# Kernel tuning notes

Hardware: AMD Instinct MI355X
Metric: run time of the kernel (lower is better)

The kernel has to match this reference:

```python
import jax, jax.numpy as jnp
import numpy as np

N_NODES = 50000
N_EDGES = 1600000
CHANNELS = 128
EXPANSION = 50
CUTOFF = 5.0
LOG2 = 0.6931471805599453


def shifted_softplus(x):
    return jax.nn.softplus(x) - LOG2


def gaussian_smearing(r, cutoff=CUTOFF, n=EXPANSION):
    # centers evenly spaced in [0, cutoff]; width set by spacing
    centers = jnp.linspace(0.0, cutoff, n, dtype=r.dtype)
    delta = centers[1] - centers[0]
    coef = 1.0 / (2.0 * delta * delta)
    d = r[:, None] - centers[None, :]          # [E, n]
    return jnp.exp(-coef * d * d)


def setup_inputs() -> dict:
    key = jax.random.key(0)
    ks = jax.random.split(key, 12)
    C, F = CHANNELS, EXPANSION

    def lin(k, fan_in, shape):
        bound = 1.0 / np.sqrt(fan_in)
        return jax.random.uniform(k, shape, jnp.float32, -bound, bound)

    return {
        "features": jax.random.normal(ks[0], (N_NODES, C), jnp.float32),
        "edge_distances": jax.random.uniform(ks[1], (N_EDGES,), jnp.float32) * CUTOFF,
        "W_lin": lin(ks[2], C, (C, C)),
        "Wf1": lin(ks[3], F, (F, C)), "bf1": lin(ks[4], F, (C,)),
        "Wf2": lin(ks[5], C, (C, C)), "bf2": lin(ks[6], C, (C,)),
        "Wm1": lin(ks[7], C, (C, C)), "bm1": lin(ks[8], C, (C,)),
        "Wm2": lin(ks[9], C, (C, C)), "bm2": lin(ks[10], C, (C,)),
        "senders": jax.random.randint(ks[11], (N_EDGES,), 0, N_NODES, jnp.int32),
        "receivers": jax.random.randint(jax.random.fold_in(key, 99), (N_EDGES,), 0, N_NODES, jnp.int32),
    }


def reference(features, edge_distances, W_lin, Wf1, bf1, Wf2, bf2,
              Wm1, bm1, Wm2, bm2, senders, receivers):
    # 1. linear transform of node features (no bias)
    h = features @ W_lin.T                                   # [N, C]
    # 2. learnable radial filter F(r_ij): Gaussian basis -> MLP
    basis = gaussian_smearing(edge_distances)                # [E, F]
    ef = shifted_softplus(basis @ Wf1 + bf1) @ Wf2 + bf2     # [E, C]
    # 3. gather neighbour features, elementwise multiply, scatter-sum
    messages = h[senders] * ef                               # [E, C]
    agg = jax.ops.segment_sum(messages, receivers, num_segments=N_NODES)  # [N, C]
    # 4. output MLP
    return shifted_softplus(agg @ Wm1 + bm1) @ Wm2 + bm2
```

## Files before the change

kernel.cpp:

```cpp
#include <hip/hip_runtime.h>
#include <hip/hip_bf16.h>
#include <math.h>

#define N_NODES 50000
#define N_EDGES 1600000
#define CH 128
#define NF 50
#define NR 16384
#define NODES_PER_BLK 8
#define CHUNK 1024
#define NB 512
#define BUCKET_NODES 98
#define CAP 3840
#define PASSA_CHUNK 4096
#define NBLK_SCAT 391
#define NBLK_TB   8192
#define NBLK_DH   782

constexpr float DELTA  = 5.0f / 49.0f;
constexpr float COEF   = 1.0f / (2.0f * DELTA * DELTA);
constexpr float LOG2_  = 0.6931471805599453f;
constexpr float RSCALE = (float)(NR - 1) / 5.0f;

typedef short  bf16x8 __attribute__((ext_vector_type(8)));
typedef float  f32x4  __attribute__((ext_vector_type(4)));
typedef unsigned short ushort_t;
typedef unsigned long long u64;

__device__ __forceinline__ float ssp(float x) {
    return fmaxf(x, 0.0f) + __logf(1.0f + __expf(-fabsf(x))) - LOG2_;
}
__device__ __forceinline__ ushort_t f2bf(float x) {
    __hip_bfloat16 b = __float2bfloat16(x);
    return *reinterpret_cast<ushort_t*>(&b);
}
__device__ __forceinline__ float bf2f(ushort_t u) {
    return __uint_as_float(((unsigned)u) << 16);
}
__device__ __forceinline__ float4 f4zero() { return make_float4(0.f, 0.f, 0.f, 0.f); }

__global__ __launch_bounds__(256) void k1_prep(const float* __restrict__ Wlin,
                                               const float* __restrict__ Wm1,
                                               const float* __restrict__ Wm2,
                                               ushort_t* __restrict__ wlhi,
                                               ushort_t* __restrict__ wllo,
                                               ushort_t* __restrict__ wm1hi,
                                               ushort_t* __restrict__ wm1lo,
                                               ushort_t* __restrict__ wm2hi,
                                               ushort_t* __restrict__ wm2lo,
                                               int* __restrict__ bcnt) {
    const int tid = threadIdx.x;
    if (blockIdx.x == 64) {
        bcnt[tid] = 0;
        bcnt[tid + 256] = 0;
        return;
    }
    int idx = blockIdx.x * 256 + tid;
    int n = idx >> 7, k = idx & 127;
    {   float w = Wlin[(size_t)n * CH + k];
        ushort_t hi = f2bf(w); wlhi[n * CH + k] = hi; wllo[n * CH + k] = f2bf(w - bf2f(hi)); }
    {   float w = Wm1[(size_t)k * CH + n];
        ushort_t hi = f2bf(w); wm1hi[n * CH + k] = hi; wm1lo[n * CH + k] = f2bf(w - bf2f(hi)); }
    {   float w = Wm2[(size_t)k * CH + n];
        ushort_t hi = f2bf(w); wm2hi[n * CH + k] = hi; wm2lo[n * CH + k] = f2bf(w - bf2f(hi)); }
}

__device__ void scatter_body(char* smem, int blk,
                             const int* __restrict__ recv,
                             const int* __restrict__ send,
                             const float* __restrict__ dist,
                             int* __restrict__ bcnt,
                             u64* __restrict__ brec) {
    int* bcur   = (int*)smem;
    int* bbaseL = bcur + NB;
    const int tid = threadIdx.x;
    for (int i = tid; i < NB; i += 256) bcur[i] = 0;
    __syncthreads();
    const int e0 = blk * PASSA_CHUNK;
#pragma unroll
    for (int i = 0; i < 16; i++) {
        int e = e0 + tid + i * 256;
        if (e < N_EDGES) atomicAdd(&bcur[recv[e] / BUCKET_NODES], 1);
    }
    __syncthreads();
    for (int i = tid; i < NB; i += 256) {
        int c = bcur[i];
        bbaseL[i] = c ? atomicAdd(&bcnt[i], c) : 0;
        bcur[i] = 0;
    }
    __syncthreads();
#pragma unroll
    for (int i = 0; i < 16; i++) {
        int e = e0 + tid + i * 256;
        if (e < N_EDGES) {
            int r = recv[e];
            int b = r / BUCKET_NODES;
            int rank = bbaseL[b] + atomicAdd(&bcur[b], 1);
            if (rank < CAP) {
                float x = fminf(dist[e] * RSCALE, (float)(NR - 1));
                int ti = __float2int_rn(x);
                u64 rec = (u64)(unsigned)(send[e] | (r << 16)) | ((u64)ti << 32);
                brec[(size_t)b * CAP + rank] = rec;
            }
        }
    }
}

__device__ void table_body(char* smem, int blk,
                           const float* __restrict__ Wf1,
                           const float* __restrict__ bf1,
                           const float* __restrict__ Wf2,
                           const float* __restrict__ bf2,
                           ushort_t* __restrict__ tabn) {
    float* bas = (float*)smem;
    float* t1  = (float*)smem + 128;
    const int tid  = threadIdx.x;
    const int half = tid >> 7, t = tid & 127;
    const int g = blk * 2 + half;
    const float r = (float)g * (5.0f / (float)(NR - 1));
    if (t < 64) {
        float v = 0.f;
        if (t < NF) { float d = r - (float)t * DELTA; v = __expf(-COEF * d * d); }
        bas[half * 64 + t] = v;
    }
    __syncthreads();
    float acc = bf1[t];
    for (int k = 0; k < NF; k++) acc = fmaf(bas[half * 64 + k], Wf1[k * CH + t], acc);
    t1[half * 128 + t] = ssp(acc);
    __syncthreads();
    float acc2 = bf2[t];
    for (int k = 0; k < CH; k++) acc2 = fmaf(t1[half * 128 + k], Wf2[k * CH + t], acc2);
    tabn[(size_t)g * CH + t] = f2bf(acc2);
}

__device__ void dense_h_body(char* smem, int blk,
                             const float* __restrict__ X,
                             const ushort_t* __restrict__ Bhi,
                             const ushort_t* __restrict__ Blo,
                             ushort_t* __restrict__ Y) {
    ushort_t (*xs)[136] = (ushort_t (*)[136])smem;
    const int tid  = threadIdx.x;
    const int row0 = blk * 64;

#pragma unroll
    for (int i = 0; i < 8; i++) {
        int idx = tid + i * 256;
        int r   = idx >> 5;
        int c4  = (idx & 31) * 4;
        float4 v = (row0 + r < N_NODES) ? *(const float4*)&X[(size_t)(row0 + r) * CH + c4]
                                        : f4zero();
        ushort4 s;
        s.x = f2bf(v.x); s.y = f2bf(v.y); s.z = f2bf(v.z); s.w = f2bf(v.w);
        *(ushort4*)&xs[r][c4] = s;
    }
    __syncthreads();

    const int lane = tid & 63;
    const int wv   = tid >> 6;
    const int row  = lane & 15;
    const int quad = lane >> 4;
    const int c0   = (2 * wv) * 16 + row;
    const int c1   = c0 + 16;

    f32x4 acc[2][4];
#pragma unroll
    for (int j = 0; j < 2; j++)
#pragma unroll
        for (int rt = 0; rt < 4; rt++) acc[j][rt] = (f32x4){0.f, 0.f, 0.f, 0.f};

#pragma unroll
    for (int kb = 0; kb < 128; kb += 32) {
        bf16x8 B0h = *(const bf16x8*)&Bhi[(size_t)c0 * CH + kb + quad * 8];
        bf16x8 B0l = *(const bf16x8*)&Blo[(size_t)c0 * CH + kb + quad * 8];
        bf16x8 B1h = *(const bf16x8*)&Bhi[(size_t)c1 * CH + kb + quad * 8];
        bf16x8 B1l = *(const bf16x8*)&Blo[(size_t)c1 * CH + kb + quad * 8];
#pragma unroll
        for (int rt = 0; rt < 4; rt++) {
            bf16x8 A = *(const bf16x8*)&xs[rt * 16 + row][kb + quad * 8];
            acc[0][rt] = __builtin_amdgcn_mfma_f32_16x16x32_bf16(A, B0l, acc[0][rt], 0, 0, 0);
            acc[0][rt] = __builtin_amdgcn_mfma_f32_16x16x32_bf16(A, B0h, acc[0][rt], 0, 0, 0);
            acc[1][rt] = __builtin_amdgcn_mfma_f32_16x16x32_bf16(A, B1l, acc[1][rt], 0, 0, 0);
            acc[1][rt] = __builtin_amdgcn_mfma_f32_16x16x32_bf16(A, B1h, acc[1][rt], 0, 0, 0);
        }
    }

#pragma unroll
    for (int j = 0; j < 2; j++) {
        int c = j ? c1 : c0;
#pragma unroll
        for (int rt = 0; rt < 4; rt++)
#pragma unroll
            for (int rg = 0; rg < 4; rg++) {
                int r = row0 + rt * 16 + quad * 4 + rg;
                if (r < N_NODES) Y[(size_t)r * CH + c] = f2bf(acc[j][rt][rg]);
            }
    }
}

__global__ __launch_bounds__(256) void k2_mega(const int* __restrict__ recv,
                                               const int* __restrict__ send,
                                               const float* __restrict__ dist,
                                               int* __restrict__ bcnt,
                                               u64* __restrict__ brec,
                                               const float* __restrict__ Wf1,
                                               const float* __restrict__ bf1,
                                               const float* __restrict__ Wf2,
                                               const float* __restrict__ bf2,
                                               ushort_t* __restrict__ tabn,
                                               const float* __restrict__ X,
                                               const ushort_t* __restrict__ wlhi,
                                               const ushort_t* __restrict__ wllo,
                                               ushort_t* __restrict__ h) {
    __shared__ __align__(16) char smem[64 * 136 * 2];
    const int blk = blockIdx.x;
    if (blk < NBLK_SCAT) {
        scatter_body(smem, blk, recv, send, dist, bcnt, brec);
    } else if (blk < NBLK_SCAT + NBLK_TB) {
        table_body(smem, blk - NBLK_SCAT, Wf1, bf1, Wf2, bf2, tabn);
    } else {
        dense_h_body(smem, blk - NBLK_SCAT - NBLK_TB, X, wlhi, wllo, h);
    }
}

__global__ __launch_bounds__(256) void bucket_sort(const int* __restrict__ bcnt,
                                                   const u64* __restrict__ brec,
                                                   unsigned* __restrict__ meta,
                                                   int* __restrict__ cursor) {
    __shared__ int sbc[NB];
    __shared__ int shist[BUCKET_NODES];
    __shared__ int sexc[BUCKET_NODES];
    __shared__ unsigned sout[CAP];
    __shared__ int sgb;
    const int b = blockIdx.x, tid = threadIdx.x;
    const int nbase = b * BUCKET_NODES;
    const int nn = min(BUCKET_NODES, N_NODES - nbase);
    if (nn <= 0) return;

    sbc[tid] = bcnt[tid];
    sbc[tid + 256] = bcnt[tid + 256];
    for (int i = tid; i < nn; i += 256) shist[i] = 0;
    __syncthreads();
    if (tid == 0) {
        int acc = 0;
        for (int i = 0; i < b; i++) acc += min(sbc[i], CAP);
        sgb = acc;
    }
    __syncthreads();
    const int gbase = sgb;
    const int m = min(sbc[b], CAP);
    const u64* my = brec + (size_t)b * CAP;

    for (int i = tid; i < m; i += 256) {
        int l = (int)((my[i] >> 16) & 0xFFFF) - nbase;
        atomicAdd(&shist[l], 1);
    }
    __syncthreads();
    if (tid == 0) {
        int acc = 0;
        for (int l = 0; l < nn; l++) { sexc[l] = acc; acc += shist[l]; }
    }
    __syncthreads();
    for (int l = tid; l < nn; l += 256)
        cursor[nbase + l] = gbase + sexc[l] + shist[l];
    __syncthreads();
    for (int i = tid; i < m; i += 256) {
        u64 rec = my[i];
        int l = (int)((rec >> 16) & 0xFFFF) - nbase;
        int rank = atomicAdd(&sexc[l], 1);
        sout[rank] = (unsigned)(rec & 0xFFFF) | ((unsigned)((rec >> 32) & 0x3FFF) << 16);
    }
    __syncthreads();
    for (int i = tid; i < m; i += 256) meta[gbase + i] = sout[i];
}

__global__ __launch_bounds__(256) void edge_gather(const int* __restrict__ cursor,
                                                   const unsigned* __restrict__ meta,
                                                   const ushort_t* __restrict__ h,
                                                   const ushort_t* __restrict__ tabn,
                                                   ushort_t* __restrict__ aggb) {
    __shared__ unsigned smeta[CHUNK];

    const int tid = threadIdx.x;
    const int n0  = blockIdx.x * NODES_PER_BLK;
    const int g   = tid >> 5;
    const int c4  = (tid & 31) * 4;
    const int n   = n0 + g;

    const int myend  = cursor[n];
    const int mybeg  = (n == 0) ? 0 : cursor[n - 1];
    const int blkbeg = (n0 == 0) ? 0 : cursor[n0 - 1];
    const int blkend = cursor[n0 + NODES_PER_BLK - 1];

    float4 macc = f4zero();

    for (int cs = blkbeg; cs < blkend; cs += CHUNK) {
        const int ce = min(cs + CHUNK, blkend);
        __syncthreads();
        for (int i = tid; i < ce - cs; i += 256) smeta[i] = meta[cs + i];
        __syncthreads();

        const int lo = max(mybeg, cs), hi = min(myend, ce);
        int e = lo;
        for (; e + 4 <= hi; e += 4) {
            int s[4], ti[4];
#pragma unroll
            for (int u = 0; u < 4; u++) {
                unsigned v = smeta[e - cs + u];
                s[u]  = (int)(v & 0xFFFF);
                ti[u] = (int)(v >> 16);
            }
            ushort4 hu[4], tn[4];
#pragma unroll
            for (int u = 0; u < 4; u++) {
                hu[u] = *(const ushort4*)&h[(size_t)s[u] * CH + c4];
                tn[u] = *(const ushort4*)&tabn[(size_t)ti[u] * CH + c4];
            }
#pragma unroll
            for (int u = 0; u < 4; u++) {
                macc.x = fmaf(bf2f(hu[u].x), bf2f(tn[u].x), macc.x);
                macc.y = fmaf(bf2f(hu[u].y), bf2f(tn[u].y), macc.y);
                macc.z = fmaf(bf2f(hu[u].z), bf2f(tn[u].z), macc.z);
                macc.w = fmaf(bf2f(hu[u].w), bf2f(tn[u].w), macc.w);
            }
        }
        for (; e < hi; e++) {
            unsigned v = smeta[e - cs];
            int s  = (int)(v & 0xFFFF);
            int ti = (int)(v >> 16);
            ushort4 hu = *(const ushort4*)&h[(size_t)s * CH + c4];
            ushort4 tn = *(const ushort4*)&tabn[(size_t)ti * CH + c4];
            macc.x = fmaf(bf2f(hu.x), bf2f(tn.x), macc.x);
            macc.y = fmaf(bf2f(hu.y), bf2f(tn.y), macc.y);
            macc.z = fmaf(bf2f(hu.z), bf2f(tn.z), macc.z);
            macc.w = fmaf(bf2f(hu.w), bf2f(tn.w), macc.w);
        }
    }

    ushort4 o;
    o.x = f2bf(macc.x); o.y = f2bf(macc.y); o.z = f2bf(macc.z); o.w = f2bf(macc.w);
    *(ushort4*)&aggb[(size_t)n * CH + c4] = o;
}

__global__ __launch_bounds__(256) void out_mlp(const ushort_t* __restrict__ AGG,
                                               const ushort_t* __restrict__ B1hi,
                                               const ushort_t* __restrict__ B1lo,
                                               const float* __restrict__ bm1,
                                               const ushort_t* __restrict__ B2hi,
                                               const ushort_t* __restrict__ B2lo,
                                               const float* __restrict__ bm2,
                                               float* __restrict__ OUT, int M) {
    __shared__ ushort_t xs[64][136];
    __shared__ ushort_t ts[64][136];
    const int tid  = threadIdx.x;
    const int row0 = blockIdx.x * 64;

#pragma unroll
    for (int i = 0; i < 4; i++) {
        int idx = tid + i * 256;
        int r   = idx >> 4;
        int c8  = (idx & 15) * 8;
        uint4 v = (row0 + r < M) ? *(const uint4*)&AGG[(size_t)(row0 + r) * CH + c8]
                                 : make_uint4(0, 0, 0, 0);
        *(uint4*)&xs[r][c8] = v;
    }
    __syncthreads();

    const int lane = tid & 63;
    const int wv   = tid >> 6;
    const int row  = lane & 15;
    const int quad = lane >> 4;
    const int c0   = (2 * wv) * 16 + row;
    const int c1   = c0 + 16;

    f32x4 acc[2][4];
#pragma unroll
    for (int j = 0; j < 2; j++)
#pragma unroll
        for (int rt = 0; rt < 4; rt++) acc[j][rt] = (f32x4){0.f, 0.f, 0.f, 0.f};

#pragma unroll
    for (int kb = 0; kb < 128; kb += 32) {
        bf16x8 B0h = *(const bf16x8*)&B1hi[(size_t)c0 * CH + kb + quad * 8];
        bf16x8 B0l = *(const bf16x8*)&B1lo[(size_t)c0 * CH + kb + quad * 8];
        bf16x8 B1h_ = *(const bf16x8*)&B1hi[(size_t)c1 * CH + kb + quad * 8];
        bf16x8 B1l_ = *(const bf16x8*)&B1lo[(size_t)c1 * CH + kb + quad * 8];
#pragma unroll
        for (int rt = 0; rt < 4; rt++) {
            bf16x8 A = *(const bf16x8*)&xs[rt * 16 + row][kb + quad * 8];
            acc[0][rt] = __builtin_amdgcn_mfma_f32_16x16x32_bf16(A, B0l, acc[0][rt], 0, 0, 0);
            acc[0][rt] = __builtin_amdgcn_mfma_f32_16x16x32_bf16(A, B0h, acc[0][rt], 0, 0, 0);
            acc[1][rt] = __builtin_amdgcn_mfma_f32_16x16x32_bf16(A, B1l_, acc[1][rt], 0, 0, 0);
            acc[1][rt] = __builtin_amdgcn_mfma_f32_16x16x32_bf16(A, B1h_, acc[1][rt], 0, 0, 0);
        }
    }
    {
        float bv[2] = { bm1[c0], bm1[c1] };
#pragma unroll
        for (int j = 0; j < 2; j++) {
            int c = j ? c1 : c0;
#pragma unroll
            for (int rt = 0; rt < 4; rt++)
#pragma unroll
                for (int rg = 0; rg < 4; rg++)
                    ts[rt * 16 + quad * 4 + rg][c] = f2bf(ssp(acc[j][rt][rg] + bv[j]));
        }
    }
    __syncthreads();

#pragma unroll
    for (int j = 0; j < 2; j++)
#pragma unroll
        for (int rt = 0; rt < 4; rt++) acc[j][rt] = (f32x4){0.f, 0.f, 0.f, 0.f};

#pragma unroll
    for (int kb = 0; kb < 128; kb += 32) {
        bf16x8 B0h = *(const bf16x8*)&B2hi[(size_t)c0 * CH + kb + quad * 8];
        bf16x8 B0l = *(const bf16x8*)&B2lo[(size_t)c0 * CH + kb + quad * 8];
        bf16x8 B1h_ = *(const bf16x8*)&B2hi[(size_t)c1 * CH + kb + quad * 8];
        bf16x8 B1l_ = *(const bf16x8*)&B2lo[(size_t)c1 * CH + kb + quad * 8];
#pragma unroll
        for (int rt = 0; rt < 4; rt++) {
            bf16x8 A = *(const bf16x8*)&ts[rt * 16 + row][kb + quad * 8];
            acc[0][rt] = __builtin_amdgcn_mfma_f32_16x16x32_bf16(A, B0l, acc[0][rt], 0, 0, 0);
            acc[0][rt] = __builtin_amdgcn_mfma_f32_16x16x32_bf16(A, B0h, acc[0][rt], 0, 0, 0);
            acc[1][rt] = __builtin_amdgcn_mfma_f32_16x16x32_bf16(A, B1l_, acc[1][rt], 0, 0, 0);
            acc[1][rt] = __builtin_amdgcn_mfma_f32_16x16x32_bf16(A, B1h_, acc[1][rt], 0, 0, 0);
        }
    }
    {
        float bv[2] = { bm2[c0], bm2[c1] };
#pragma unroll
        for (int j = 0; j < 2; j++) {
            int c = j ? c1 : c0;
#pragma unroll
            for (int rt = 0; rt < 4; rt++)
#pragma unroll
                for (int rg = 0; rg < 4; rg++) {
                    int r = row0 + rt * 16 + quad * 4 + rg;
                    if (r < M) OUT[(size_t)r * CH + c] = acc[j][rt][rg] + bv[j];
                }
        }
    }
}

extern "C" void kernel_launch(void* const* d_in, const int* in_sizes, int n_in,
                              void* d_out, int out_size, void* d_ws, size_t ws_size,
                              hipStream_t stream) {
    const float* features = (const float*)d_in[0];
    const float* dist     = (const float*)d_in[1];
    const float* W_lin    = (const float*)d_in[2];
    const float* Wf1      = (const float*)d_in[3];
    const float* bf1      = (const float*)d_in[4];
    const float* Wf2      = (const float*)d_in[5];
    const float* bf2      = (const float*)d_in[6];
    const float* Wm1      = (const float*)d_in[7];
    const float* bm1      = (const float*)d_in[8];
    const float* Wm2      = (const float*)d_in[9];
    const float* bm2      = (const float*)d_in[10];
    const int* senders    = (const int*)d_in[11];
    const int* receivers  = (const int*)d_in[12];
    float* out = (float*)d_out;

    u64* brec       = (u64*)d_ws;
    ushort_t* aggb  = (ushort_t*)d_ws;
    ushort_t* h     = (ushort_t*)(brec + (size_t)NB * CAP);
    unsigned* meta  = (unsigned*)(h + (size_t)N_NODES * CH);
    ushort_t* tabn  = (ushort_t*)(meta + N_EDGES);
    int* cursor     = (int*)(tabn + (size_t)NR * CH);
    int* bcnt       = cursor + N_NODES;
    ushort_t* wlhi  = (ushort_t*)(bcnt + NB);
    ushort_t* wllo  = wlhi  + CH * CH;
    ushort_t* wm1hi = wllo  + CH * CH;
    ushort_t* wm1lo = wm1hi + CH * CH;
    ushort_t* wm2hi = wm1lo + CH * CH;
    ushort_t* wm2lo = wm2hi + CH * CH;

    k1_prep<<<65, 256, 0, stream>>>(W_lin, Wm1, Wm2,
                                    wlhi, wllo, wm1hi, wm1lo, wm2hi, wm2lo, bcnt);

    k2_mega<<<NBLK_SCAT + NBLK_TB + NBLK_DH, 256, 0, stream>>>(
        receivers, senders, dist, bcnt, brec,
        Wf1, bf1, Wf2, bf2, tabn,
        features, wlhi, wllo, h);

    bucket_sort<<<NB, 256, 0, stream>>>(bcnt, brec, meta, cursor);

    edge_gather<<<N_NODES / NODES_PER_BLK, 256, 0, stream>>>(cursor, meta, h, tabn, aggb);

    out_mlp<<<NBLK_DH, 256, 0, stream>>>(aggb, wm1hi, wm1lo, bm1,
                                         wm2hi, wm2lo, bm2, out, N_NODES);
}
```

Before: 294.5 us.

## Fuse bucket sort with edge gather and build radial table via MFMA

Merges the bucket sort and the edge gather into one kernel, so each bucket's sorted edge list stays in shared memory and is consumed directly. This removes the global meta and cursor arrays and one kernel launch. The radial filter table is halved to 8192 entries and computed with bf16 MFMA tiles of 64 rows per block instead of scalar FMA loops. Wf2 is split into hi/lo bf16 for accuracy and Wf1 is cast to bf16, which gives a coarser table and some precision loss. Only 512 blocks now do the gather, each handling 98 nodes, which may reduce parallelism.

```diff
diff --git a/kernel.cpp b/kernel.cpp
--- a/kernel.cpp
+++ b/kernel.cpp
@@ -6,15 +6,13 @@
 #define N_EDGES 1600000
 #define CH 128
 #define NF 50
-#define NR 16384
-#define NODES_PER_BLK 8
-#define CHUNK 1024
+#define NR 8192
 #define NB 512
 #define BUCKET_NODES 98
-#define CAP 3840
+#define CAP 3584
 #define PASSA_CHUNK 4096
 #define NBLK_SCAT 391
-#define NBLK_TB   8192
+#define NBLK_TB   128
 #define NBLK_DH   782
 
 constexpr float DELTA  = 5.0f / 49.0f;
@@ -42,12 +40,17 @@
 __global__ __launch_bounds__(256) void k1_prep(const float* __restrict__ Wlin,
                                                const float* __restrict__ Wm1,
                                                const float* __restrict__ Wm2,
+                                               const float* __restrict__ Wf1,
+                                               const float* __restrict__ Wf2,
                                                ushort_t* __restrict__ wlhi,
                                                ushort_t* __restrict__ wllo,
                                                ushort_t* __restrict__ wm1hi,
                                                ushort_t* __restrict__ wm1lo,
                                                ushort_t* __restrict__ wm2hi,
                                                ushort_t* __restrict__ wm2lo,
+                                               ushort_t* __restrict__ wf1t,
+                                               ushort_t* __restrict__ wf2hi,
+                                               ushort_t* __restrict__ wf2lo,
                                                int* __restrict__ bcnt) {
     const int tid = threadIdx.x;
     if (blockIdx.x == 64) {
@@ -63,6 +66,9 @@
         ushort_t hi = f2bf(w); wm1hi[n * CH + k] = hi; wm1lo[n * CH + k] = f2bf(w - bf2f(hi)); }
     {   float w = Wm2[(size_t)k * CH + n];
         ushort_t hi = f2bf(w); wm2hi[n * CH + k] = hi; wm2lo[n * CH + k] = f2bf(w - bf2f(hi)); }
+    if (k < 64) wf1t[n * 64 + k] = (k < NF) ? f2bf(Wf1[k * CH + n]) : (ushort_t)0;
+    {   float w = Wf2[(size_t)k * CH + n];
+        ushort_t hi = f2bf(w); wf2hi[n * CH + k] = hi; wf2lo[n * CH + k] = f2bf(w - bf2f(hi)); }
 }
 
 __device__ void scatter_body(char* smem, int blk,
@@ -107,30 +113,103 @@
 }
 
 __device__ void table_body(char* smem, int blk,
-                           const float* __restrict__ Wf1,
                            const float* __restrict__ bf1,
-                           const float* __restrict__ Wf2,
                            const float* __restrict__ bf2,
+                           const ushort_t* __restrict__ wf1t,
+                           const ushort_t* __restrict__ wf2hi,
+                           const ushort_t* __restrict__ wf2lo,
                            ushort_t* __restrict__ tabn) {
-    float* bas = (float*)smem;
-    float* t1  = (float*)smem + 128;
-    const int tid  = threadIdx.x;
-    const int half = tid >> 7, t = tid & 127;
-    const int g = blk * 2 + half;
-    const float r = (float)g * (5.0f / (float)(NR - 1));
-    if (t < 64) {
-        float v = 0.f;
-        if (t < NF) { float d = r - (float)t * DELTA; v = __expf(-COEF * d * d); }
-        bas[half * 64 + t] = v;
-    }
-    __syncthreads();
-    float acc = bf1[t];
-    for (int k = 0; k < NF; k++) acc = fmaf(bas[half * 64 + k], Wf1[k * CH + t], acc);
-    t1[half * 128 + t] = ssp(acc);
-    __syncthreads();
-    float acc2 = bf2[t];
-    for (int k = 0; k < CH; k++) acc2 = fmaf(t1[half * 128 + k], Wf2[k * CH + t], acc2);
-    tabn[(size_t)g * CH + t] = f2bf(acc2);
+    ushort_t (*basis)[72] = (ushort_t (*)[72])smem;
+    ushort_t (*t1s)[136]  = (ushort_t (*)[136])(smem + 64 * 72 * 2);
+    const int tid = threadIdx.x;
+    const int g0  = blk * 64;
+
+    for (int i = tid; i < 64 * 64; i += 256) {
+        int e = i >> 6, k = i & 63;
+        float val = 0.f;
+        if (k < NF) {
+            float r = (float)(g0 + e) * (5.0f / (float)(NR - 1));
+            float d = r - (float)k * DELTA;
+            val = __expf(-COEF * d * d);
+        }
+        basis[e][k] = f2bf(val);
+    }
+    __syncthreads();
+
+    const int lane = tid & 63;
+    const int wv   = tid >> 6;
+    const int row  = lane & 15;
+    const int quad = lane >> 4;
+    const int c0   = (2 * wv) * 16 + row;
+    const int c1   = c0 + 16;
+
+    f32x4 acc[2][4];
+#pragma unroll
+    for (int j = 0; j < 2; j++)
+#pragma unroll
+        for (int rt = 0; rt < 4; rt++) acc[j][rt] = (f32x4){0.f, 0.f, 0.f, 0.f};
+
+#pragma unroll
+    for (int kb = 0; kb < 64; kb += 32) {
+        bf16x8 B0 = *(const bf16x8*)&wf1t[c0 * 64 + kb + quad * 8];
+        bf16x8 B1 = *(const bf16x8*)&wf1t[c1 * 64 + kb + quad * 8];
+#pragma unroll
+        for (int rt = 0; rt < 4; rt++) {
+            bf16x8 A = *(const bf16x8*)&basis[rt * 16 + row][kb + quad * 8];
+            acc[0][rt] = __builtin_amdgcn_mfma_f32_16x16x32_bf16(A, B0, acc[0][rt], 0, 0, 0);
+            acc[1][rt] = __builtin_amdgcn_mfma_f32_16x16x32_bf16(A, B1, acc[1][rt], 0, 0, 0);
+        }
+    }
+    {
+        float b1v[2] = { bf1[c0], bf1[c1] };
+#pragma unroll
+        for (int j = 0; j < 2; j++) {
+            int c = j ? c1 : c0;
+#pragma unroll
+            for (int rt = 0; rt < 4; rt++)
+#pragma unroll
+                for (int rg = 0; rg < 4; rg++) {
+                    int e = rt * 16 + quad * 4 + rg;
+                    t1s[e][c] = f2bf(ssp(acc[j][rt][rg] + b1v[j]));
+                }
+        }
+    }
+    __syncthreads();
+
+#pragma unroll
+    for (int j = 0; j < 2; j++)
+#pragma unroll
+        for (int rt = 0; rt < 4; rt++) acc[j][rt] = (f32x4){0.f, 0.f, 0.f, 0.f};
+
+#pragma unroll
+    for (int kb = 0; kb < 128; kb += 32) {
+        bf16x8 B0h = *(const bf16x8*)&wf2hi[c0 * CH + kb + quad * 8];
+        bf16x8 B0l = *(const bf16x8*)&wf2lo[c0 * CH + kb + quad * 8];
+        bf16x8 B1h = *(const bf16x8*)&wf2hi[c1 * CH + kb + quad * 8];
+        bf16x8 B1l = *(const bf16x8*)&wf2lo[c1 * CH + kb + quad * 8];
+#pragma unroll
+        for (int rt = 0; rt < 4; rt++) {
+            bf16x8 A = *(const bf16x8*)&t1s[rt * 16 + row][kb + quad * 8];
+            acc[0][rt] = __builtin_amdgcn_mfma_f32_16x16x32_bf16(A, B0l, acc[0][rt], 0, 0, 0);
+            acc[0][rt] = __builtin_amdgcn_mfma_f32_16x16x32_bf16(A, B0h, acc[0][rt], 0, 0, 0);
+            acc[1][rt] = __builtin_amdgcn_mfma_f32_16x16x32_bf16(A, B1l, acc[1][rt], 0, 0, 0);
+            acc[1][rt] = __builtin_amdgcn_mfma_f32_16x16x32_bf16(A, B1h, acc[1][rt], 0, 0, 0);
+        }
+    }
+    {
+        float b2v[2] = { bf2[c0], bf2[c1] };
+#pragma unroll
+        for (int j = 0; j < 2; j++) {
+            int c = j ? c1 : c0;
+#pragma unroll
+            for (int rt = 0; rt < 4; rt++)
+#pragma unroll
+                for (int rg = 0; rg < 4; rg++) {
+                    int g = g0 + rt * 16 + quad * 4 + rg;
+                    tabn[(size_t)g * CH + c] = f2bf(acc[j][rt][rg] + b2v[j]);
+                }
+        }
+    }
 }
 
 __device__ void dense_h_body(char* smem, int blk,
@@ -202,54 +281,45 @@
                                                const float* __restrict__ dist,
                                                int* __restrict__ bcnt,
                                                u64* __restrict__ brec,
-                                               const float* __restrict__ Wf1,
                                                const float* __restrict__ bf1,
-                                               const float* __restrict__ Wf2,
                                                const float* __restrict__ bf2,
+                                               const ushort_t* __restrict__ wf1t,
+                                               const ushort_t* __restrict__ wf2hi,
+                                               const ushort_t* __restrict__ wf2lo,
                                                ushort_t* __restrict__ tabn,
                                                const float* __restrict__ X,
                                                const ushort_t* __restrict__ wlhi,
                                                const ushort_t* __restrict__ wllo,
                                                ushort_t* __restrict__ h) {
-    __shared__ __align__(16) char smem[64 * 136 * 2];
+    __shared__ __align__(16) char smem[64 * 72 * 2 + 64 * 136 * 2];
     const int blk = blockIdx.x;
     if (blk < NBLK_SCAT) {
         scatter_body(smem, blk, recv, send, dist, bcnt, brec);
     } else if (blk < NBLK_SCAT + NBLK_TB) {
-        table_body(smem, blk - NBLK_SCAT, Wf1, bf1, Wf2, bf2, tabn);
+        table_body(smem, blk - NBLK_SCAT, bf1, bf2, wf1t, wf2hi, wf2lo, tabn);
     } else {
         dense_h_body(smem, blk - NBLK_SCAT - NBLK_TB, X, wlhi, wllo, h);
     }
 }
 
-__global__ __launch_bounds__(256) void bucket_sort(const int* __restrict__ bcnt,
+__global__ __launch_bounds__(256) void sort_gather(const int* __restrict__ bcnt,
                                                    const u64* __restrict__ brec,
-                                                   unsigned* __restrict__ meta,
-                                                   int* __restrict__ cursor) {
-    __shared__ int sbc[NB];
+                                                   const ushort_t* __restrict__ h,
+                                                   const ushort_t* __restrict__ tabn,
+                                                   ushort_t* __restrict__ aggb) {
     __shared__ int shist[BUCKET_NODES];
+    __shared__ int sbeg[BUCKET_NODES];
     __shared__ int sexc[BUCKET_NODES];
     __shared__ unsigned sout[CAP];
-    __shared__ int sgb;
     const int b = blockIdx.x, tid = threadIdx.x;
     const int nbase = b * BUCKET_NODES;
     const int nn = min(BUCKET_NODES, N_NODES - nbase);
     if (nn <= 0) return;
-
-    sbc[tid] = bcnt[tid];
-    sbc[tid + 256] = bcnt[tid + 256];
+    const int m = min(bcnt[b], CAP);
+    const u64* my = brec + (size_t)b * CAP;
+
     for (int i = tid; i < nn; i += 256) shist[i] = 0;
     __syncthreads();
-    if (tid == 0) {
-        int acc = 0;
-        for (int i = 0; i < b; i++) acc += min(sbc[i], CAP);
-        sgb = acc;
-    }
-    __syncthreads();
-    const int gbase = sgb;
-    const int m = min(sbc[b], CAP);
-    const u64* my = brec + (size_t)b * CAP;
-
     for (int i = tid; i < m; i += 256) {
         int l = (int)((my[i] >> 16) & 0xFFFF) - nbase;
         atomicAdd(&shist[l], 1);
@@ -260,8 +330,7 @@
         for (int l = 0; l < nn; l++) { sexc[l] = acc; acc += shist[l]; }
     }
     __syncthreads();
-    for (int l = tid; l < nn; l += 256)
-        cursor[nbase + l] = gbase + sexc[l] + shist[l];
+    for (int l = tid; l < nn; l += 256) sbeg[l] = sexc[l];
     __syncthreads();
     for (int i = tid; i < m; i += 256) {
         u64 rec = my[i];
@@ -270,42 +339,18 @@
         sout[rank] = (unsigned)(rec & 0xFFFF) | ((unsigned)((rec >> 32) & 0x3FFF) << 16);
     }
     __syncthreads();
-    for (int i = tid; i < m; i += 256) meta[gbase + i] = sout[i];
-}
-
-__global__ __launch_bounds__(256) void edge_gather(const int* __restrict__ cursor,
-                                                   const unsigned* __restrict__ meta,
-                                                   const ushort_t* __restrict__ h,
-                                                   const ushort_t* __restrict__ tabn,
-                                                   ushort_t* __restrict__ aggb) {
-    __shared__ unsigned smeta[CHUNK];
-
-    const int tid = threadIdx.x;
-    const int n0  = blockIdx.x * NODES_PER_BLK;
-    const int g   = tid >> 5;
-    const int c4  = (tid & 31) * 4;
-    const int n   = n0 + g;
-
-    const int myend  = cursor[n];
-    const int mybeg  = (n == 0) ? 0 : cursor[n - 1];
-    const int blkbeg = (n0 == 0) ? 0 : cursor[n0 - 1];
-    const int blkend = cursor[n0 + NODES_PER_BLK - 1];
-
-    float4 macc = f4zero();
-
-    for (int cs = blkbeg; cs < blkend; cs += CHUNK) {
-        const int ce = min(cs + CHUNK, blkend);
-        __syncthreads();
-        for (int i = tid; i < ce - cs; i += 256) smeta[i] = meta[cs + i];
-        __syncthreads();
-
-        const int lo = max(mybeg, cs), hi = min(myend, ce);
-        int e = lo;
-        for (; e + 4 <= hi; e += 4) {
+
+    const int g  = tid >> 5;
+    const int c4 = (tid & 31) * 4;
+    for (int l = g; l < nn; l += 8) {
+        const int beg = sbeg[l], end = sbeg[l] + shist[l];
+        float4 macc = f4zero();
+        int e = beg;
+        for (; e + 4 <= end; e += 4) {
             int s[4], ti[4];
 #pragma unroll
             for (int u = 0; u < 4; u++) {
-                unsigned v = smeta[e - cs + u];
+                unsigned v = sout[e + u];
                 s[u]  = (int)(v & 0xFFFF);
                 ti[u] = (int)(v >> 16);
             }
@@ -323,8 +368,8 @@
                 macc.w = fmaf(bf2f(hu[u].w), bf2f(tn[u].w), macc.w);
             }
         }
-        for (; e < hi; e++) {
-            unsigned v = smeta[e - cs];
+        for (; e < end; e++) {
+            unsigned v = sout[e];
             int s  = (int)(v & 0xFFFF);
             int ti = (int)(v >> 16);
             ushort4 hu = *(const ushort4*)&h[(size_t)s * CH + c4];
@@ -334,11 +379,10 @@
             macc.z = fmaf(bf2f(hu.z), bf2f(tn.z), macc.z);
             macc.w = fmaf(bf2f(hu.w), bf2f(tn.w), macc.w);
         }
-    }
-
-    ushort4 o;
-    o.x = f2bf(macc.x); o.y = f2bf(macc.y); o.z = f2bf(macc.z); o.w = f2bf(macc.w);
-    *(ushort4*)&aggb[(size_t)n * CH + c4] = o;
+        ushort4 o;
+        o.x = f2bf(macc.x); o.y = f2bf(macc.y); o.z = f2bf(macc.z); o.w = f2bf(macc.w);
+        *(ushort4*)&aggb[(size_t)(nbase + l) * CH + c4] = o;
+    }
 }
 
 __global__ __launch_bounds__(256) void out_mlp(const ushort_t* __restrict__ AGG,
@@ -462,30 +506,30 @@
     float* out = (float*)d_out;
 
     u64* brec       = (u64*)d_ws;
-    ushort_t* aggb  = (ushort_t*)d_ws;
     ushort_t* h     = (ushort_t*)(brec + (size_t)NB * CAP);
-    unsigned* meta  = (unsigned*)(h + (size_t)N_NODES * CH);
-    ushort_t* tabn  = (ushort_t*)(meta + N_EDGES);
-    int* cursor     = (int*)(tabn + (size_t)NR * CH);
-    int* bcnt       = cursor + N_NODES;
+    ushort_t* aggb  = h + (size_t)N_NODES * CH;
+    ushort_t* tabn  = aggb + (size_t)N_NODES * CH;
+    int* bcnt       = (int*)(tabn + (size_t)NR * CH);
     ushort_t* wlhi  = (ushort_t*)(bcnt + NB);
     ushort_t* wllo  = wlhi  + CH * CH;
     ushort_t* wm1hi = wllo  + CH * CH;
     ushort_t* wm1lo = wm1hi + CH * CH;
     ushort_t* wm2hi = wm1lo + CH * CH;
     ushort_t* wm2lo = wm2hi + CH * CH;
-
-    k1_prep<<<65, 256, 0, stream>>>(W_lin, Wm1, Wm2,
-                                    wlhi, wllo, wm1hi, wm1lo, wm2hi, wm2lo, bcnt);
+    ushort_t* wf1t  = wm2lo + CH * CH;
+    ushort_t* wf2hi = wf1t  + CH * 64;
+    ushort_t* wf2lo = wf2hi + CH * CH;
+
+    k1_prep<<<65, 256, 0, stream>>>(W_lin, Wm1, Wm2, Wf1, Wf2,
+                                    wlhi, wllo, wm1hi, wm1lo, wm2hi, wm2lo,
+                                    wf1t, wf2hi, wf2lo, bcnt);
 
     k2_mega<<<NBLK_SCAT + NBLK_TB + NBLK_DH, 256, 0, stream>>>(
         receivers, senders, dist, bcnt, brec,
-        Wf1, bf1, Wf2, bf2, tabn,
+        bf1, bf2, wf1t, wf2hi, wf2lo, tabn,
         features, wlhi, wllo, h);
 
-    bucket_sort<<<NB, 256, 0, stream>>>(bcnt, brec, meta, cursor);
-
-    edge_gather<<<N_NODES / NODES_PER_BLK, 256, 0, stream>>>(cursor, meta, h, tabn, aggb);
+    sort_gather<<<NB, 256, 0, stream>>>(bcnt, brec, h, tabn, aggb);
 
     out_mlp<<<NBLK_DH, 256, 0, stream>>>(aggb, wm1hi, wm1lo, bm1,
                                          wm2hi, wm2lo, bm2, out, N_NODES);
```

New measurement: 266.3 us. 1.11x faster.
